# Kernel optimization log

Measured on AMD Instinct MI355X. Metric: run time of the kernel, lower is better.

## Reference

```python
import jax, jax.numpy as jnp
import numpy as np

CONF_TH = 0.25   # default conf_thresh in non_max_suppression
NMS_TH = 0.35    # default nms_thresh


def setup_inputs() -> dict:
    key = jax.random.key(0)
    # [N, C=5+num_classes, H, W]
    preds = jax.random.normal(key, (64, 85, 32, 32), dtype=jnp.float32)
    return {"preds": preds}


def _decode(preds):
    """Faithful box decode: [N,C,H,W] -> [N, H*W, 6] (x1,y1,x2,y2,score,cls)."""
    N, C, H, W = preds.shape
    p = jnp.transpose(preds, (0, 2, 3, 1))           # [N,H,W,C]
    pobj = p[..., 0]
    preg = p[..., 1:5]
    pcls = p[..., 5:]
    score = pobj * jnp.max(pcls, axis=-1)             # obj * max-class
    cls = jax.lax.stop_gradient(jnp.argmax(pcls, axis=-1).astype(preds.dtype))
    gy, gx = jnp.meshgrid(jnp.arange(H, dtype=preds.dtype),
                          jnp.arange(W, dtype=preds.dtype), indexing="ij")
    bw = jax.nn.sigmoid(preg[..., 2])
    bh = jax.nn.sigmoid(preg[..., 3])
    bcx = (jnp.tanh(preg[..., 0]) + gx) / W
    bcy = (jnp.tanh(preg[..., 1]) + gy) / H
    x1 = bcx - 0.5 * bw
    y1 = bcy - 0.5 * bh
    x2 = bcx + 0.5 * bw
    y2 = bcy + 0.5 * bh
    bboxes = jnp.stack([x1, y1, x2, y2, score, cls], axis=-1)  # [N,H,W,6]
    return bboxes.reshape(N, H * W, 6)


def _iou_matrix(boxes):
    """[M,4] xyxy -> [M,M] pairwise IoU."""
    x1, y1, x2, y2 = boxes[:, 0], boxes[:, 1], boxes[:, 2], boxes[:, 3]
    area = (x2 - x1) * (y2 - y1)
    iw = jnp.clip(jnp.minimum(x2[:, None], x2[None, :]) - jnp.maximum(x1[:, None], x1[None, :]), 0.0)
    ih = jnp.clip(jnp.minimum(y2[:, None], y2[None, :]) - jnp.maximum(y1[:, None], y1[None, :]), 0.0)
    inter = iw * ih
    return inter / (area[:, None] + area[None, :] - inter + 1e-9)


def _nms_single(bb):
    """Greedy class-aware NMS on one image's [M,6] boxes.
    Equivalent to: filter score>CONF_TH then torchvision.batched_nms.
    Returns keep mask [M] in the original box order (fixed shape)."""
    M = bb.shape[0]
    order = jnp.argsort(-bb[:, 4])                    # descending score
    b = bb[order]
    iou = _iou_matrix(b[:, :4])
    same_cls = b[:, 5][:, None] == b[:, 5][None, :]
    supp_mat = (iou > NMS_TH) & same_cls              # [M,M]
    valid_s = b[:, 4] > CONF_TH

    def body(i, keep):
        suppressed = jnp.any(keep & supp_mat[i])
        return keep.at[i].set(valid_s[i] & ~suppressed)

    keep_s = jax.lax.fori_loop(0, M, body, jnp.zeros((M,), jnp.bool_))
    # scatter back to original order
    return jnp.zeros((M,), jnp.bool_).at[order].set(keep_s)


def reference(preds):
    bboxes = _decode(preds)                # [N, HW, 6]
    keep = jax.vmap(_nms_single)(bboxes)   # [N, HW] bool keep mask
    return bboxes, keep
```

## Files before the change

kernel.cpp:

```cpp
#include <hip/hip_runtime.h>
#include <math.h>

#define NIMG 64
#define HW   1024
#define NCH  85
#define NCLS 80
#define NW   16
#define CPW  5
#define CONF_TH 0.25f
#define NMS_TH  0.35f

__device__ __forceinline__ float fast_tanh(float x) {
  float e = __expf(2.0f * x);
  return 1.0f - 2.0f * __builtin_amdgcn_rcpf(e + 1.0f);
}
__device__ __forceinline__ float fast_sigmoid(float x) {
  return __builtin_amdgcn_rcpf(1.0f + __expf(-x));
}

template <int CL0, int NC>
__device__ __forceinline__ void quarter_argmax(const float* __restrict__ bp,
                                               float4& mv, int4& mi) {
  float4 v = *(const float4*)(bp + (size_t)CL0 * HW);
  float b0 = v.x, b1 = v.y, b2 = v.z, b3 = v.w;
  int i0 = CL0 - 5, i1 = i0, i2 = i0, i3 = i0;
#pragma unroll
  for (int c = 1; c < NC; ++c) {
    float4 u = *(const float4*)(bp + (size_t)(CL0 + c) * HW);
    int ci = CL0 - 5 + c;
    if (u.x > b0) { b0 = u.x; i0 = ci; }
    if (u.y > b1) { b1 = u.y; i1 = ci; }
    if (u.z > b2) { b2 = u.z; i2 = ci; }
    if (u.w > b3) { b3 = u.w; i3 = ci; }
  }
  mv = make_float4(b0, b1, b2, b3);
  mi = make_int4(i0, i1, i2, i3);
}

__global__ __launch_bounds__(1024) void fused_kernel(const float* __restrict__ preds,
                                                     float* __restrict__ out,
                                                     float* __restrict__ keepOut) {
  int n = blockIdx.x;
  int t = threadIdx.x;
  int q  = t >> 8;
  int pg = t & 255;
  int wv   = t >> 6;
  int lane = t & 63;

  __shared__ float sx1[HW], sy1[HW], sx2[HW], sy2[HW], sarea[HW], sscore[HW];
  __shared__ int scls[HW];
  __shared__ float pmaxv[4][HW];
  __shared__ int   pmaxi[4][HW];
  __shared__ float sobj[HW];
  __shared__ float sreg[4][HW];
  __shared__ unsigned short mlist[NW][HW];
  __shared__ unsigned short ssort[NW][64];
  __shared__ unsigned long long wflags[NW][32];

  const float* bp = preds + (size_t)n * (NCH * HW) + 4 * pg;
  float4 mv; int4 mi;
  if (q == 0) {
    float4 vobj = *(const float4*)(bp);
    ((float4*)sobj)[pg] = vobj;
#pragma unroll
    for (int r = 0; r < 4; ++r) {
      float4 vr = *(const float4*)(bp + (size_t)(1 + r) * HW);
      ((float4*)&sreg[r][0])[pg] = vr;
    }
    quarter_argmax<5, 16>(bp, mv, mi);
  } else if (q == 1) {
    quarter_argmax<21, 21>(bp, mv, mi);
  } else if (q == 2) {
    quarter_argmax<42, 21>(bp, mv, mi);
  } else {
    quarter_argmax<63, 22>(bp, mv, mi);
  }
  ((float4*)&pmaxv[q][0])[pg] = mv;
  ((int4*)&pmaxi[q][0])[pg] = mi;
  __syncthreads();

  float pobj = sobj[t];
  float tx = sreg[0][t], ty = sreg[1][t], tw = sreg[2][t], th = sreg[3][t];
  float best = pmaxv[0][t]; int bc = pmaxi[0][t];
#pragma unroll
  for (int qq = 1; qq < 4; ++qq) {
    float v = pmaxv[qq][t];
    if (v > best) { best = v; bc = pmaxi[qq][t]; }
  }
  float score = pobj * best;

  float gx = (float)(t & 31);
  float gy = (float)(t >> 5);
  float bcx = (fast_tanh(tx) + gx) * 0.03125f;
  float bcy = (fast_tanh(ty) + gy) * 0.03125f;
  float bw = fast_sigmoid(tw);
  float bh = fast_sigmoid(th);

  float x1 = bcx - 0.5f * bw, y1 = bcy - 0.5f * bh;
  float x2 = bcx + 0.5f * bw, y2 = bcy + 0.5f * bh;

  size_t gb = (size_t)n * HW + t;
  float2* ob = (float2*)(out + gb * 6);
  ob[0] = make_float2(x1, y1);
  ob[1] = make_float2(x2, y2);
  ob[2] = make_float2(score, (float)bc);

  sx1[t] = x1; sy1[t] = y1; sx2[t] = x2; sy2[t] = y2;
  sarea[t] = (x2 - x1) * (y2 - y1);
  sscore[t] = score;
  scls[t] = bc;
  keepOut[gb] = 0.0f;
  __syncthreads();

  int   cls_r[16];
  float sc_r[16];
#pragma unroll
  for (int k = 0; k < 16; ++k) {
    int p = (k << 6) | lane;
    cls_r[k] = scls[p];
    sc_r[k]  = sscore[p];
  }

  for (int ci = 0; ci < CPW; ++ci) {
    int c = wv * CPW + ci;

    int m = 0;
#pragma unroll
    for (int k = 0; k < 16; ++k) {
      bool pred = (cls_r[k] == c) && (sc_r[k] > CONF_TH);
      unsigned long long mask = __ballot(pred);
      while (mask) {
        int l = __ffsll((unsigned long long)mask) - 1;
        mask &= mask - 1;
        if (lane == 0) mlist[wv][m] = (unsigned short)((k << 6) | l);
        ++m;
      }
    }
    if (m == 0) continue;

    if (m <= 64) {
      int pj = 0; float scj = 0.0f; int rj = 0;
      bool active = (lane < m);
      if (active) { pj = mlist[wv][lane]; scj = sscore[pj]; }
      for (int i = 0; i < m; ++i) {
        int pi = mlist[wv][i];
        float si = sscore[pi];
        if (active) rj += (si > scj) || (si == scj && pi < pj);
      }
      if (active) ssort[wv][rj] = (unsigned short)pj;

      float kx1 = 0, ky1 = 0, kx2 = 0, ky2 = 0, kar = 0;
      if (active) {
        int qb = ssort[wv][lane];
        kx1 = sx1[qb]; ky1 = sy1[qb]; kx2 = sx2[qb]; ky2 = sy2[qb]; kar = sarea[qb];
      }

      unsigned long long kept = 0ull;
      for (int a = 0; a < m; ++a) {
        int qa = ssort[wv][a];
        float ax1 = sx1[qa], ay1 = sy1[qa], ax2 = sx2[qa], ay2 = sy2[qa];
        float aar = sarea[qa];
        bool sup = false;
        if (lane < a && ((kept >> lane) & 1ull)) {
          float iw = fminf(ax2, kx2) - fmaxf(ax1, kx1);
          float ih = fminf(ay2, ky2) - fmaxf(ay1, ky1);
          iw = fmaxf(iw, 0.0f);
          ih = fmaxf(ih, 0.0f);
          float inter = iw * ih;
          float iou = inter / (aar + kar - inter + 1e-9f);
          sup = iou > NMS_TH;
        }
        unsigned long long v = __ballot(sup);
        if (v == 0ull) {
          kept |= (1ull << a);
          if (lane == 0) keepOut[(size_t)n * HW + qa] = 1.0f;
        }
      }
    } else {
      if (lane == 0) {
        for (int i = 0; i < 32; ++i) wflags[wv][i] = 0ull;
        for (int a = 0; a < m; ++a) {
          int bj = -1; float bs = 0.0f; int bpx = 0;
          for (int j = 0; j < m; ++j) {
            if ((wflags[wv][j >> 6] >> (j & 63)) & 1ull) continue;
            int pj2 = mlist[wv][j];
            float sj2 = sscore[pj2];
            if (bj < 0 || sj2 > bs || (sj2 == bs && pj2 < bpx)) { bj = j; bs = sj2; bpx = pj2; }
          }
          wflags[wv][bj >> 6] |= 1ull << (bj & 63);
          float cx1 = sx1[bpx], cy1 = sy1[bpx], cx2 = sx2[bpx], cy2 = sy2[bpx];
          float car = sarea[bpx];
          bool kp = true;
          for (int j = 0; j < m && kp; ++j) {
            if (!((wflags[wv][16 + (j >> 6)] >> (j & 63)) & 1ull)) continue;
            int pj2 = mlist[wv][j];
            float iw = fminf(cx2, sx2[pj2]) - fmaxf(cx1, sx1[pj2]);
            float ih = fminf(cy2, sy2[pj2]) - fmaxf(cy1, sy1[pj2]);
            iw = fmaxf(iw, 0.0f);
            ih = fmaxf(ih, 0.0f);
            float inter = iw * ih;
            float iou = inter / (car + sarea[pj2] - inter + 1e-9f);
            if (iou > NMS_TH) kp = false;
          }
          if (kp) {
            wflags[wv][16 + (bj >> 6)] |= 1ull << (bj & 63);
            keepOut[(size_t)n * HW + bpx] = 1.0f;
          }
        }
      }
    }
  }
}

extern "C" void kernel_launch(void* const* d_in, const int* in_sizes, int n_in,
                              void* d_out, int out_size, void* d_ws, size_t ws_size,
                              hipStream_t stream) {
  const float* preds = (const float*)d_in[0];
  float* out = (float*)d_out;
  float* keepOut = out + (size_t)NIMG * HW * 6;

  fused_kernel<<<NIMG, HW, 0, stream>>>(preds, out, keepOut);
}
```

Before: 86.51 us.

## Split fused decode+NMS into a wide decode kernel and a per-image NMS kernel

Moves box decoding into its own kernel launched with 256 blocks of 256 threads instead of 64 blocks of 1024, so the 22 MB read of predictions is spread across more CUs. The NMS kernel then re-reads the decoded boxes from global memory into shared memory. It also replaces the serial per-bit mask extraction when building candidate lists with a parallel popcount-prefix write, and reads class and score from shared memory instead of caching them in registers. In exchange it adds a second launch and a global round-trip of the decoded boxes.

New measurement: 87.68 us. About the same (+1.4%).

```diff
diff --git a/kernel.cpp b/kernel.cpp
--- a/kernel.cpp
+++ b/kernel.cpp
@@ -18,75 +18,42 @@
   return __builtin_amdgcn_rcpf(1.0f + __expf(-x));
 }
 
-template <int CL0, int NC>
-__device__ __forceinline__ void quarter_argmax(const float* __restrict__ bp,
-                                               float4& mv, int4& mi) {
-  float4 v = *(const float4*)(bp + (size_t)CL0 * HW);
-  float b0 = v.x, b1 = v.y, b2 = v.z, b3 = v.w;
-  int i0 = CL0 - 5, i1 = i0, i2 = i0, i3 = i0;
-#pragma unroll
-  for (int c = 1; c < NC; ++c) {
-    float4 u = *(const float4*)(bp + (size_t)(CL0 + c) * HW);
-    int ci = CL0 - 5 + c;
-    if (u.x > b0) { b0 = u.x; i0 = ci; }
-    if (u.y > b1) { b1 = u.y; i1 = ci; }
-    if (u.z > b2) { b2 = u.z; i2 = ci; }
-    if (u.w > b3) { b3 = u.w; i3 = ci; }
-  }
-  mv = make_float4(b0, b1, b2, b3);
-  mi = make_int4(i0, i1, i2, i3);
-}
-
-__global__ __launch_bounds__(1024) void fused_kernel(const float* __restrict__ preds,
+__global__ __launch_bounds__(256) void decode_kernel(const float* __restrict__ preds,
                                                      float* __restrict__ out,
                                                      float* __restrict__ keepOut) {
-  int n = blockIdx.x;
-  int t = threadIdx.x;
-  int q  = t >> 8;
-  int pg = t & 255;
-  int wv   = t >> 6;
-  int lane = t & 63;
-
-  __shared__ float sx1[HW], sy1[HW], sx2[HW], sy2[HW], sarea[HW], sscore[HW];
-  __shared__ int scls[HW];
-  __shared__ float pmaxv[4][HW];
-  __shared__ int   pmaxi[4][HW];
-  __shared__ float sobj[HW];
-  __shared__ float sreg[4][HW];
-  __shared__ unsigned short mlist[NW][HW];
-  __shared__ unsigned short ssort[NW][64];
-  __shared__ unsigned long long wflags[NW][32];
-
-  const float* bp = preds + (size_t)n * (NCH * HW) + 4 * pg;
-  float4 mv; int4 mi;
-  if (q == 0) {
-    float4 vobj = *(const float4*)(bp);
-    ((float4*)sobj)[pg] = vobj;
+  int gid = blockIdx.x * 256 + threadIdx.x;
+  int n = gid >> 10;
+  int t = gid & 1023;
+  const float* bp = preds + (size_t)n * (NCH * HW) + t;
+
+  float pobj = bp[0];
+  float tx = bp[(size_t)1 * HW];
+  float ty = bp[(size_t)2 * HW];
+  float tw = bp[(size_t)3 * HW];
+  float th = bp[(size_t)4 * HW];
+
+  float b0, b1, b2, b3;
+  int i0, i1, i2, i3;
+  b0 = bp[(size_t)(5 +  0) * HW]; i0 =  0;
+  b1 = bp[(size_t)(5 + 20) * HW]; i1 = 20;
+  b2 = bp[(size_t)(5 + 40) * HW]; i2 = 40;
+  b3 = bp[(size_t)(5 + 60) * HW]; i3 = 60;
 #pragma unroll
-    for (int r = 0; r < 4; ++r) {
-      float4 vr = *(const float4*)(bp + (size_t)(1 + r) * HW);
-      ((float4*)&sreg[r][0])[pg] = vr;
-    }
-    quarter_argmax<5, 16>(bp, mv, mi);
-  } else if (q == 1) {
-    quarter_argmax<21, 21>(bp, mv, mi);
-  } else if (q == 2) {
-    quarter_argmax<42, 21>(bp, mv, mi);
-  } else {
-    quarter_argmax<63, 22>(bp, mv, mi);
+  for (int c = 1; c < 20; ++c) {
+    float v0 = bp[(size_t)(5 +  0 + c) * HW];
+    float v1 = bp[(size_t)(5 + 20 + c) * HW];
+    float v2 = bp[(size_t)(5 + 40 + c) * HW];
+    float v3 = bp[(size_t)(5 + 60 + c) * HW];
+    if (v0 > b0) { b0 = v0; i0 =  0 + c; }
+    if (v1 > b1) { b1 = v1; i1 = 20 + c; }
+    if (v2 > b2) { b2 = v2; i2 = 40 + c; }
+    if (v3 > b3) { b3 = v3; i3 = 60 + c; }
   }
-  ((float4*)&pmaxv[q][0])[pg] = mv;
-  ((int4*)&pmaxi[q][0])[pg] = mi;
-  __syncthreads();
-
-  float pobj = sobj[t];
-  float tx = sreg[0][t], ty = sreg[1][t], tw = sreg[2][t], th = sreg[3][t];
-  float best = pmaxv[0][t]; int bc = pmaxi[0][t];
-#pragma unroll
-  for (int qq = 1; qq < 4; ++qq) {
-    float v = pmaxv[qq][t];
-    if (v > best) { best = v; bc = pmaxi[qq][t]; }
-  }
+  float best = b0; int bc = i0;
+  if (b1 > best) { best = b1; bc = i1; }
+  if (b2 > best) { best = b2; bc = i2; }
+  if (b3 > best) { best = b3; bc = i3; }
+
   float score = pobj * best;
 
   float gx = (float)(t & 31);
@@ -99,27 +66,37 @@
   float x1 = bcx - 0.5f * bw, y1 = bcy - 0.5f * bh;
   float x2 = bcx + 0.5f * bw, y2 = bcy + 0.5f * bh;
 
-  size_t gb = (size_t)n * HW + t;
-  float2* ob = (float2*)(out + gb * 6);
+  float2* ob = (float2*)(out + (size_t)gid * 6);
   ob[0] = make_float2(x1, y1);
   ob[1] = make_float2(x2, y2);
   ob[2] = make_float2(score, (float)bc);
 
-  sx1[t] = x1; sy1[t] = y1; sx2[t] = x2; sy2[t] = y2;
-  sarea[t] = (x2 - x1) * (y2 - y1);
-  sscore[t] = score;
-  scls[t] = bc;
-  keepOut[gb] = 0.0f;
+  keepOut[gid] = 0.0f;
+}
+
+__global__ __launch_bounds__(1024) void nms_kernel(const float* __restrict__ boxes,
+                                                   float* __restrict__ keepOut) {
+  int n = blockIdx.x;
+  int t = threadIdx.x;
+  int wv   = t >> 6;
+  int lane = t & 63;
+
+  __shared__ float sx1[HW], sy1[HW], sx2[HW], sy2[HW], sarea[HW], sscore[HW];
+  __shared__ int scls[HW];
+  __shared__ unsigned short mlist[NW][HW];
+  __shared__ unsigned short ssort[NW][64];
+  __shared__ unsigned long long wflags[NW][32];
+
+  size_t gb = (size_t)n * HW + t;
+  const float2* ib = (const float2*)(boxes + gb * 6);
+  float2 a01 = ib[0];
+  float2 a23 = ib[1];
+  float2 a45 = ib[2];
+  sx1[t] = a01.x; sy1[t] = a01.y; sx2[t] = a23.x; sy2[t] = a23.y;
+  sarea[t] = (a23.x - a01.x) * (a23.y - a01.y);
+  sscore[t] = a45.x;
+  scls[t] = (int)a45.y;
   __syncthreads();
-
-  int   cls_r[16];
-  float sc_r[16];
-#pragma unroll
-  for (int k = 0; k < 16; ++k) {
-    int p = (k << 6) | lane;
-    cls_r[k] = scls[p];
-    sc_r[k]  = sscore[p];
-  }
 
   for (int ci = 0; ci < CPW; ++ci) {
     int c = wv * CPW + ci;
@@ -127,20 +104,20 @@
     int m = 0;
 #pragma unroll
     for (int k = 0; k < 16; ++k) {
-      bool pred = (cls_r[k] == c) && (sc_r[k] > CONF_TH);
+      int p = (k << 6) | lane;
+      bool pred = (scls[p] == c) && (sscore[p] > CONF_TH);
       unsigned long long mask = __ballot(pred);
-      while (mask) {
-        int l = __ffsll((unsigned long long)mask) - 1;
-        mask &= mask - 1;
-        if (lane == 0) mlist[wv][m] = (unsigned short)((k << 6) | l);
-        ++m;
-      }
+      if (pred) {
+        int prefix = __popcll(mask & ((1ull << lane) - 1ull));
+        mlist[wv][m + prefix] = (unsigned short)p;
+      }
+      m += __popcll(mask);
     }
     if (m == 0) continue;
 
     if (m <= 64) {
+      bool active = (lane < m);
       int pj = 0; float scj = 0.0f; int rj = 0;
-      bool active = (lane < m);
       if (active) { pj = mlist[wv][lane]; scj = sscore[pj]; }
       for (int i = 0; i < m; ++i) {
         int pi = mlist[wv][i];
@@ -219,5 +196,6 @@
   float* out = (float*)d_out;
   float* keepOut = out + (size_t)NIMG * HW * 6;
 
-  fused_kernel<<<NIMG, HW, 0, stream>>>(preds, out, keepOut);
-}
+  decode_kernel<<<NIMG * HW / 256, 256, 0, stream>>>(preds, out, keepOut);
+  nms_kernel<<<NIMG, HW, 0, stream>>>(out, keepOut);
+}
```
